# Kernel optimization log

Measured on AMD Instinct MI355X. Metric: run time of the kernel, lower is better.

Reference implementation:

```python
import jax, jax.numpy as jnp
import numpy as np

B, T, C = 8, 2048, 1024   # batch, seq_len, n_embd
HS = 1024                 # head_size


def setup_inputs() -> dict:
    key = jax.random.key(0)
    k1, k2, k3, k4 = jax.random.split(key, 4)
    x = jax.random.normal(k1, (B, T, C), dtype=jnp.float32)
    k_wei = jax.random.normal(k2, (C, HS), dtype=jnp.float32) * (C ** -0.5)
    q_wei = jax.random.normal(k3, (C, HS), dtype=jnp.float32) * (C ** -0.5)
    v_wei = jax.random.normal(k4, (C, HS), dtype=jnp.float32) * (C ** -0.5)
    mask = jnp.tril(jnp.ones((T, T), dtype=bool))  # causal tril, block_size >= T
    return {"x": x, "k_wei": k_wei, "q_wei": q_wei, "v_wei": v_wei, "mask": mask}


def reference(x, k_wei, q_wei, v_wei, mask):
    Bb, Tt, Cc = x.shape
    k = x @ k_wei                                   # [B,T,HS]
    q = x @ q_wei                                   # [B,T,HS]
    v = x @ v_wei                                   # [B,T,HS]
    # NOTE: source scales by C**-0.5 where C = n_embd (input channels)
    wei = jnp.einsum('bqh,bkh->bqk', q, k) * (Cc ** -0.5)  # [B,T,T]
    wei = jnp.where(mask[:Tt, :Tt], wei, -jnp.inf)
    wei = jax.nn.softmax(wei, axis=-1)
    out = wei @ v                                   # [B,T,HS]
    return out
```

## Files before the change

kernel.cpp:

```cpp
#include <hip/hip_runtime.h>
#include <hip/hip_bf16.h>
#include <stdint.h>

typedef __attribute__((ext_vector_type(4))) float f32x4;
typedef __attribute__((ext_vector_type(8))) short s16x8;

#define BARRIER() asm volatile("s_barrier" ::: "memory")
#define WAITV4()  asm volatile("s_waitcnt vmcnt(4)" ::: "memory")
#define WAITV0()  asm volatile("s_waitcnt vmcnt(0)" ::: "memory")
#define LGKM0()   asm volatile("s_waitcnt lgkmcnt(0)" ::: "memory")
#define MFMA(a, b, c) __builtin_amdgcn_mfma_f32_16x16x32_bf16((a), (b), (c), 0, 0, 0)

__device__ __forceinline__ ushort f2bf(float f) {
  union { float f; uint32_t u; } v; v.f = f;
  uint32_t r = v.u + 0x7FFFu + ((v.u >> 16) & 1u);
  return (ushort)(r >> 16);
}

__device__ __forceinline__ void gload_lds16(const ushort* g, short* l) {
  __builtin_amdgcn_global_load_lds(
      (const __attribute__((address_space(1))) uint32_t*)g,
      (__attribute__((address_space(3))) uint32_t*)l, 16, 0, 0);
}

__device__ __forceinline__ int xcd_swz(int flat, int q) {
  return (flat & 7) * q + (flat >> 3);
}

__device__ __forceinline__ void stage128(const ushort* __restrict__ g, int ld,
                                         int row0, int k0, short* lbase, int tid) {
  const int w  = tid >> 6;
  const int l  = tid & 63;
  const int lr = l >> 3;
  const int ls = l & 7;
  const ushort* gp = g + (size_t)(row0 + lr) * ld + k0 + ((ls ^ lr) << 3);
  short* lp = lbase + l * 8;
#pragma unroll
  for (int i = 0; i < 4; ++i) {
    const int R0 = w * 32 + i * 8;
    gload_lds16(gp + (size_t)R0 * ld, lp + R0 * 64);
  }
}

__device__ __forceinline__ void gstep(
    const ushort* __restrict__ A, int lda, const ushort* __restrict__ Bt, int ldb,
    int m0, int n0, int nk, int X, short* Ac, short* Bs,
    int tid, int s0, int aro, int bro, f32x4 acc[4][4], bool skipw)
{
  if (X + 1 < nk) { WAITV4(); } else { WAITV0(); }
  BARRIER();

  s16x8 b[4][2], a[4][2];
  if (!skipw) {
#pragma unroll
    for (int ni = 0; ni < 4; ++ni) {
      b[ni][0] = *(const s16x8*)(Bs + bro + ni * 1024 + s0);
      b[ni][1] = *(const s16x8*)(Bs + bro + ni * 1024 + (s0 ^ 32));
    }
#pragma unroll
    for (int mi = 0; mi < 4; ++mi) {
      a[mi][0] = *(const s16x8*)(Ac + aro + mi * 1024 + s0);
      a[mi][1] = *(const s16x8*)(Ac + aro + mi * 1024 + (s0 ^ 32));
    }
    __builtin_amdgcn_s_setprio(1);
#pragma unroll
    for (int mi = 0; mi < 2; ++mi)
#pragma unroll
      for (int ni = 0; ni < 4; ++ni) {
        acc[mi][ni] = MFMA(a[mi][0], b[ni][0], acc[mi][ni]);
        acc[mi][ni] = MFMA(a[mi][1], b[ni][1], acc[mi][ni]);
      }
    __builtin_amdgcn_s_setprio(0);
  }

  LGKM0();
  BARRIER();
  if (X + 1 < nk) stage128(Bt, ldb, n0, (X + 1) * 64, Bs, tid);
  if (X + 2 < nk) stage128(A, lda, m0, (X + 2) * 64, Ac, tid);
  if (!skipw) {
    __builtin_amdgcn_s_setprio(1);
#pragma unroll
    for (int mi = 0; mi < 2; ++mi)
#pragma unroll
      for (int ni = 0; ni < 4; ++ni) {
        acc[2 + mi][ni] = MFMA(a[2 + mi][0], b[ni][0], acc[2 + mi][ni]);
        acc[2 + mi][ni] = MFMA(a[2 + mi][1], b[ni][1], acc[2 + mi][ni]);
      }
    __builtin_amdgcn_s_setprio(0);
  }
}

__device__ __forceinline__ void gemm_core(
    const ushort* __restrict__ A, int lda, const ushort* __restrict__ Bt, int ldb,
    int m0, int n0, int nk, short* lds, f32x4 acc[4][4], bool skipw = false)
{
  const int tid  = threadIdx.x;
  const int lane = tid & 63, wid = tid >> 6;
  const int wr = wid >> 1, wc = wid & 1;
  const int fr = lane & 15, kg = lane >> 4;
  const int s0  = (kg ^ (fr & 7)) << 3;
  const int aro = (wr * 64 + fr) * 64;
  const int bro = (wc * 64 + fr) * 64;

  short* Ab0 = lds;
  short* Ab1 = lds + 8192;
  short* Bs  = lds + 16384;

#pragma unroll
  for (int i = 0; i < 4; ++i)
#pragma unroll
    for (int j = 0; j < 4; ++j)
      acc[i][j] = (f32x4){0.f, 0.f, 0.f, 0.f};

  stage128(A, lda, m0, 0, Ab0, tid);
  stage128(Bt, ldb, n0, 0, Bs, tid);
  if (nk > 1) stage128(A, lda, m0, 64, Ab1, tid);

#pragma unroll 1
  for (int X = 0; X < nk; X += 2) {
    gstep(A, lda, Bt, ldb, m0, n0, nk, X,     Ab0, Bs, tid, s0, aro, bro, acc, skipw);
    gstep(A, lda, Bt, ldb, m0, n0, nk, X + 1, Ab1, Bs, tid, s0, aro, bro, acc, skipw);
  }
}

__global__ void cvt_x(const float* __restrict__ x, ushort* __restrict__ xb)
{
  const size_t i = (size_t)(blockIdx.x * 256 + threadIdx.x) * 8;
  const f32x4 t0 = *(const f32x4*)(x + i);
  const f32x4 t1 = *(const f32x4*)(x + i + 4);
  uint4 pk;
  pk.x = (uint32_t)f2bf(t0[0]) | ((uint32_t)f2bf(t0[1]) << 16);
  pk.y = (uint32_t)f2bf(t0[2]) | ((uint32_t)f2bf(t0[3]) << 16);
  pk.z = (uint32_t)f2bf(t1[0]) | ((uint32_t)f2bf(t1[1]) << 16);
  pk.w = (uint32_t)f2bf(t1[2]) | ((uint32_t)f2bf(t1[3]) << 16);
  *(uint4*)(xb + i) = pk;
}

__global__ void cvt_w(const float* __restrict__ kw, const float* __restrict__ qw,
                      const float* __restrict__ vw, ushort* __restrict__ wt)
{
  __shared__ float t[32][33];
  const float* w = (blockIdx.z == 0) ? qw : (blockIdx.z == 1) ? kw : vw;
  const int n0 = blockIdx.x * 32, k0 = blockIdx.y * 32;
  t[threadIdx.y][threadIdx.x] = w[(size_t)(k0 + threadIdx.y) * 1024 + n0 + threadIdx.x];
  __syncthreads();
  wt[(size_t)blockIdx.z * 1048576 + (size_t)(n0 + threadIdx.y) * 1024 + k0 + threadIdx.x] =
      f2bf(t[threadIdx.x][threadIdx.y]);
}

__global__ __launch_bounds__(256) void gemm_qkv_impl(
    const ushort* __restrict__ xb, const ushort* __restrict__ wt,
    ushort* __restrict__ q, ushort* __restrict__ k, ushort* __restrict__ vT)
{
  extern __shared__ short lds[];
  const int flat = blockIdx.x + 24 * blockIdx.y;
  const int xcd = flat & 7, c = flat >> 3;
  const int mloc = c / 6, nloc = c - mloc * 6;
  const int m0 = ((xcd & 1) * 64 + mloc) * 128;
  const int n0 = ((xcd >> 1) * 6 + nloc) * 128;
  f32x4 acc[4][4];
  gemm_core(xb, 1024, wt, 1024, m0, n0, 16, lds, acc);

  const int tid  = threadIdx.x;
  const int lane = tid & 63;
  const int wid  = tid >> 6;
  const int wr = wid >> 1, wc = wid & 1;
  const int q4 = (lane >> 4) << 2;
  const int fr = lane & 15;
  const int z  = n0 >> 10;

  if (z < 2) {
    ushort* o = (z == 0) ? q : k;
    const int cb = (n0 & 1023) + wc * 64 + fr;
#pragma unroll
    for (int mi = 0; mi < 4; ++mi)
#pragma unroll
      for (int ni = 0; ni < 4; ++ni)
#pragma unroll
        for (int j = 0; j < 4; ++j) {
          const int r = m0 + wr * 64 + mi * 16 + q4 + j;
          o[(size_t)r * 1024 + cb + ni * 16] = f2bf(acc[mi][ni][j]);
        }
  } else {
    __syncthreads();
    ushort* tr = (ushort*)lds;
#pragma unroll
    for (int mi = 0; mi < 4; ++mi)
#pragma unroll
      for (int ni = 0; ni < 4; ++ni)
#pragma unroll
        for (int j = 0; j < 4; ++j) {
          const int cl = wc * 64 + ni * 16 + fr;
          const int rl = wr * 64 + mi * 16 + q4 + j;
          tr[cl * 136 + rl] = f2bf(acc[mi][ni][j]);
        }
    __syncthreads();
    const int cl   = tid >> 1;
    const int half = tid & 1;
    const ushort* src = tr + cl * 136 + half * 64;
    ushort* dst = vT + ((size_t)(m0 >> 11) * 1024 + (n0 & 1023) + cl) * 2048
                     + (m0 & 2047) + half * 64;
#pragma unroll
    for (int i = 0; i < 8; ++i)
      *(s16x8*)(dst + i * 8) = *(const s16x8*)(src + i * 8);
  }
}

__global__ __launch_bounds__(256) void gemm_sp(
    const ushort* __restrict__ q, const ushort* __restrict__ k,
    ushort* __restrict__ P, float* __restrict__ sums)
{
  extern __shared__ short lds[];
  const int nf = xcd_swz(blockIdx.x + 136 * blockIdx.z, 136);
  const int t  = nf % 136;
  const int b  = nf / 136;
  int qt = (int)((sqrtf(8.0f * (float)t + 1.0f) - 1.0f) * 0.5f);
  while ((qt + 1) * (qt + 2) / 2 <= t) ++qt;
  while (qt * (qt + 1) / 2 > t) --qt;
  const int kt = t - qt * (qt + 1) / 2;

  const int tid  = threadIdx.x;
  const int lane = tid & 63, wid = tid >> 6;
  const int wr = wid >> 1, wc = wid & 1;
  const int diag = (kt == qt);
  const bool skipw = diag && (wr == 0) && (wc == 1);

  f32x4 acc[4][4];
  const ushort* qb = q + (size_t)b * (2048 * 1024);
  const ushort* kb = k + (size_t)b * (2048 * 1024);
  gemm_core(qb, 1024, kb, 1024, qt * 128, kt * 128, 16, lds, acc, skipw);
  __syncthreads();
  float* rowsum = (float*)lds;

  const int q4 = (lane >> 4) << 2;
  const int fr = lane & 15;
  ushort* Pb = P + ((size_t)b << 22);

#pragma unroll
  for (int mi = 0; mi < 4; ++mi)
#pragma unroll
    for (int j = 0; j < 4; ++j) {
      const int rloc = wr * 64 + mi * 16 + q4 + j;
      const int rg   = qt * 128 + rloc;
      float s = 0.f;
#pragma unroll
      for (int ni = 0; ni < 4; ++ni) {
        const int cg = kt * 128 + wc * 64 + ni * 16 + fr;
        float e = __expf(acc[mi][ni][j] * 0.03125f - 10.f);
        if (diag && cg > rg) e = 0.f;
        s += e;
        Pb[(size_t)rg * 2048 + cg] = f2bf(e);
      }
#pragma unroll
      for (int m = 1; m < 16; m <<= 1) s += __shfl_xor(s, m);
      if (fr == 0) rowsum[wc * 128 + rloc] = s;
    }
  __syncthreads();
  if (tid < 128) {
    const float tot = rowsum[tid] + rowsum[128 + tid];
    atomicAdd(&sums[b * 2048 + qt * 128 + tid], tot);
  }
}

__global__ __launch_bounds__(256) void gemm_pv(
    const ushort* __restrict__ P, const ushort* __restrict__ vT,
    const float* __restrict__ sums, float* __restrict__ out)
{
  extern __shared__ short lds[];
  const int nf = xcd_swz(blockIdx.x + 8 * (blockIdx.y + 16 * blockIdx.z), 128);
  const int ht = nf & 7, qt = (nf >> 3) & 15, b = nf >> 7;
  f32x4 acc[4][4];
  const ushort* Pb = P  + ((size_t)b << 22);
  const ushort* Vb = vT + (size_t)b * (1024 * 2048);
  gemm_core(Pb, 2048, Vb, 2048, qt * 128, ht * 128, (qt + 1) * 2, lds, acc);

  float* ob = out + (size_t)b * 2097152;
  const int lane = threadIdx.x & 63;
  const int wid = threadIdx.x >> 6;
  const int wr = wid >> 1, wc = wid & 1;
  const int r0 = qt * 128 + wr * 64 + ((lane >> 4) << 2);
  const int c0 = ht * 128 + wc * 64 + (lane & 15);
#pragma unroll
  for (int mi = 0; mi < 4; ++mi)
#pragma unroll
    for (int j = 0; j < 4; ++j) {
      const int r = r0 + mi * 16 + j;
      const float inv = 1.0f / sums[b * 2048 + r];
#pragma unroll
      for (int ni = 0; ni < 4; ++ni)
        ob[(size_t)r * 1024 + (c0 + ni * 16)] = acc[mi][ni][j] * inv;
    }
}

extern "C" void kernel_launch(void* const* d_in, const int* in_sizes, int n_in,
                              void* d_out, int out_size, void* d_ws, size_t ws_size,
                              hipStream_t stream)
{
  const float* x  = (const float*)d_in[0];
  const float* kw = (const float*)d_in[1];
  const float* qw = (const float*)d_in[2];
  const float* vw = (const float*)d_in[3];
  float* out = (float*)d_out;
  char* ws = (char*)d_ws;

  ushort* xb   = (ushort*)ws;
  ushort* P    = (ushort*)ws;
  float*  sums = (float*)(ws + 67108864);
  ushort* wt   = (ushort*)(ws + 67174400);
  ushort* q    = (ushort*)(ws + 73465856);
  ushort* k    = (ushort*)(ws + 107020288);
  ushort* vT   = (ushort*)(ws + 140574720);

  const int LDSB = 49152;
  hipMemsetAsync(sums, 0, 8 * 2048 * sizeof(float), stream);
  cvt_x<<<8192, 256, 0, stream>>>(x, xb);
  cvt_w<<<dim3(32, 32, 3), dim3(32, 32), 0, stream>>>(kw, qw, vw, wt);
  gemm_qkv_impl<<<dim3(24, 128), 256, LDSB, stream>>>(xb, wt, q, k, vT);
  gemm_sp<<<dim3(136, 1, 8), 256, LDSB, stream>>>(q, k, P, sums);
  gemm_pv<<<dim3(8, 16, 8), 256, LDSB, stream>>>(P, vT, sums, out);
}
```

Measured before the change: 245.4 us.

## Fuse fp32-to-bf16 conversion of x into QKV GEMM A-tile loading

Drops the separate cvt_x kernel. The QKV GEMM now loads fp32 x directly into registers, converts it with the packed v_cvt_pk_bf16_f32 instruction, and writes bf16 into swizzled LDS double buffers. The loads are software-pipelined across the MFMA halves with explicit vmcnt waits. This removes one launch and the bf16 x round-trip through memory, but each GEMM tile now reads 2x more A bytes (fp32), and x is re-read across 24 column tiles, with higher register pressure.

```diff
diff --git a/kernel.cpp b/kernel.cpp
--- a/kernel.cpp
+++ b/kernel.cpp
@@ -6,6 +6,8 @@
 typedef __attribute__((ext_vector_type(8))) short s16x8;
 
 #define BARRIER() asm volatile("s_barrier" ::: "memory")
+#define WAITV12() asm volatile("s_waitcnt vmcnt(12)" ::: "memory")
+#define WAITV8()  asm volatile("s_waitcnt vmcnt(8)" ::: "memory")
 #define WAITV4()  asm volatile("s_waitcnt vmcnt(4)" ::: "memory")
 #define WAITV0()  asm volatile("s_waitcnt vmcnt(0)" ::: "memory")
 #define LGKM0()   asm volatile("s_waitcnt lgkmcnt(0)" ::: "memory")
@@ -15,6 +17,12 @@
   union { float f; uint32_t u; } v; v.f = f;
   uint32_t r = v.u + 0x7FFFu + ((v.u >> 16) & 1u);
   return (ushort)(r >> 16);
+}
+
+__device__ __forceinline__ uint32_t pk2(float lo, float hi) {
+  uint32_t r;
+  asm("v_cvt_pk_bf16_f32 %0, %1, %2" : "=v"(r) : "v"(lo), "v"(hi));
+  return r;
 }
 
 __device__ __forceinline__ void gload_lds16(const ushort* g, short* l) {
@@ -42,6 +50,7 @@
   }
 }
 
+
 __device__ __forceinline__ void gstep(
     const ushort* __restrict__ A, int lda, const ushort* __restrict__ Bt, int ldb,
     int m0, int n0, int nk, int X, short* Ac, short* Bs,
@@ -123,19 +132,6 @@
   }
 }
 
-__global__ void cvt_x(const float* __restrict__ x, ushort* __restrict__ xb)
-{
-  const size_t i = (size_t)(blockIdx.x * 256 + threadIdx.x) * 8;
-  const f32x4 t0 = *(const f32x4*)(x + i);
-  const f32x4 t1 = *(const f32x4*)(x + i + 4);
-  uint4 pk;
-  pk.x = (uint32_t)f2bf(t0[0]) | ((uint32_t)f2bf(t0[1]) << 16);
-  pk.y = (uint32_t)f2bf(t0[2]) | ((uint32_t)f2bf(t0[3]) << 16);
-  pk.z = (uint32_t)f2bf(t1[0]) | ((uint32_t)f2bf(t1[1]) << 16);
-  pk.w = (uint32_t)f2bf(t1[2]) | ((uint32_t)f2bf(t1[3]) << 16);
-  *(uint4*)(xb + i) = pk;
-}
-
 __global__ void cvt_w(const float* __restrict__ kw, const float* __restrict__ qw,
                       const float* __restrict__ vw, ushort* __restrict__ wt)
 {
@@ -148,8 +144,78 @@
       f2bf(t[threadIdx.x][threadIdx.y]);
 }
 
+
+#define ALOAD(rg, k0)                                                         \
+  {                                                                           \
+    const float* xp = x + (size_t)(m0 + lr) * 1024 + (k0) + ((ls ^ lr) << 3); \
+    _Pragma("unroll")                                                         \
+    for (int i = 0; i < 4; ++i) {                                             \
+      rg[2 * i]     = *(const f32x4*)(xp + (size_t)(w * 32 + i * 8) * 1024);  \
+      rg[2 * i + 1] = *(const f32x4*)(xp + (size_t)(w * 32 + i * 8) * 1024 + 4); \
+    }                                                                         \
+  }
+
+#define AWRITE(rg, Ab)                                                        \
+  {                                                                           \
+    _Pragma("unroll")                                                         \
+    for (int i = 0; i < 4; ++i) {                                             \
+      uint4 p;                                                                \
+      p.x = pk2(rg[2 * i][0], rg[2 * i][1]);                                  \
+      p.y = pk2(rg[2 * i][2], rg[2 * i][3]);                                  \
+      p.z = pk2(rg[2 * i + 1][0], rg[2 * i + 1][1]);                          \
+      p.w = pk2(rg[2 * i + 1][2], rg[2 * i + 1][3]);                          \
+      *(uint4*)((Ab) + ((size_t)(w * 32 + i * 8 + lr) * 64 + ls * 8)) = p;    \
+    }                                                                         \
+  }
+
+#define QSTEP(X, AbR, AbW, rCur, rNext)                                       \
+  {                                                                           \
+    s16x8 b[4][2], a[4][2];                                                   \
+    _Pragma("unroll")                                                         \
+    for (int ni = 0; ni < 4; ++ni) {                                          \
+      b[ni][0] = *(const s16x8*)(Bs + bro + ni * 1024 + s0);                  \
+      b[ni][1] = *(const s16x8*)(Bs + bro + ni * 1024 + (s0 ^ 32));           \
+    }                                                                         \
+    _Pragma("unroll")                                                         \
+    for (int mi = 0; mi < 4; ++mi) {                                          \
+      a[mi][0] = *(const s16x8*)((AbR) + aro + mi * 1024 + s0);               \
+      a[mi][1] = *(const s16x8*)((AbR) + aro + mi * 1024 + (s0 ^ 32));        \
+    }                                                                         \
+    __builtin_amdgcn_s_setprio(1);                                            \
+    _Pragma("unroll")                                                         \
+    for (int mi = 0; mi < 2; ++mi)                                            \
+      _Pragma("unroll")                                                       \
+      for (int ni = 0; ni < 4; ++ni) {                                        \
+        acc[mi][ni] = MFMA(a[mi][0], b[ni][0], acc[mi][ni]);                  \
+        acc[mi][ni] = MFMA(a[mi][1], b[ni][1], acc[mi][ni]);                  \
+      }                                                                       \
+    __builtin_amdgcn_s_setprio(0);                                            \
+    LGKM0();                                                                  \
+    BARRIER();                                                                \
+    if ((X) + 1 < 16) stage128(wt, 1024, n0, ((X) + 1) * 64, Bs, tid);        \
+    if ((X) + 2 < 16) ALOAD(rNext, ((X) + 2) * 64);                           \
+    if ((X) + 1 < 16) {                                                       \
+      if ((X) + 2 < 16) { WAITV12(); } else { WAITV4(); }                     \
+      AWRITE(rCur, AbW);                                                      \
+    }                                                                         \
+    __builtin_amdgcn_s_setprio(1);                                            \
+    _Pragma("unroll")                                                         \
+    for (int mi = 0; mi < 2; ++mi)                                            \
+      _Pragma("unroll")                                                       \
+      for (int ni = 0; ni < 4; ++ni) {                                        \
+        acc[2 + mi][ni] = MFMA(a[2 + mi][0], b[ni][0], acc[2 + mi][ni]);      \
+        acc[2 + mi][ni] = MFMA(a[2 + mi][1], b[ni][1], acc[2 + mi][ni]);      \
+      }                                                                       \
+    __builtin_amdgcn_s_setprio(0);                                            \
+    if ((X) + 1 < 16) {                                                       \
+      if ((X) + 2 < 16) { WAITV8(); } else { WAITV0(); }                      \
+      LGKM0();                                                                \
+      BARRIER();                                                              \
+    }                                                                         \
+  }
+
 __global__ __launch_bounds__(256) void gemm_qkv_impl(
-    const ushort* __restrict__ xb, const ushort* __restrict__ wt,
+    const float* __restrict__ x, const ushort* __restrict__ wt,
     ushort* __restrict__ q, ushort* __restrict__ k, ushort* __restrict__ vT)
 {
   extern __shared__ short lds[];
@@ -158,15 +224,44 @@
   const int mloc = c / 6, nloc = c - mloc * 6;
   const int m0 = ((xcd & 1) * 64 + mloc) * 128;
   const int n0 = ((xcd >> 1) * 6 + nloc) * 128;
+
+  const int tid  = threadIdx.x;
+  const int lane = tid & 63, wid = tid >> 6;
+  const int wr = wid >> 1, wc = wid & 1;
+  const int fr = lane & 15, kg = lane >> 4;
+  const int s0  = (kg ^ (fr & 7)) << 3;
+  const int aro = (wr * 64 + fr) * 64;
+  const int bro = (wc * 64 + fr) * 64;
+  const int w = tid >> 6, l = tid & 63, lr = l >> 3, ls = l & 7;
+
+  short* Ab0 = lds;
+  short* Ab1 = lds + 8192;
+  short* Bs  = lds + 16384;
+
   f32x4 acc[4][4];
-  gemm_core(xb, 1024, wt, 1024, m0, n0, 16, lds, acc);
-
-  const int tid  = threadIdx.x;
-  const int lane = tid & 63;
-  const int wid  = tid >> 6;
-  const int wr = wid >> 1, wc = wid & 1;
+#pragma unroll
+  for (int i = 0; i < 4; ++i)
+#pragma unroll
+    for (int j = 0; j < 4; ++j)
+      acc[i][j] = (f32x4){0.f, 0.f, 0.f, 0.f};
+
+  f32x4 rP[8], rQ[8];
+  ALOAD(rP, 0);
+  stage128(wt, 1024, n0, 0, Bs, tid);
+  ALOAD(rQ, 64);
+  WAITV12();
+  AWRITE(rP, Ab0);
+  WAITV8();
+  LGKM0();
+  BARRIER();
+
+#pragma unroll 1
+  for (int X = 0; X < 16; X += 2) {
+    QSTEP(X,     Ab0, Ab1, rQ, rP);
+    QSTEP(X + 1, Ab1, Ab0, rP, rQ);
+  }
+
   const int q4 = (lane >> 4) << 2;
-  const int fr = lane & 15;
   const int z  = n0 >> 10;
 
   if (z < 2) {
@@ -303,7 +398,6 @@
   float* out = (float*)d_out;
   char* ws = (char*)d_ws;
 
-  ushort* xb   = (ushort*)ws;
   ushort* P    = (ushort*)ws;
   float*  sums = (float*)(ws + 67108864);
   ushort* wt   = (ushort*)(ws + 67174400);
@@ -313,9 +407,8 @@
 
   const int LDSB = 49152;
   hipMemsetAsync(sums, 0, 8 * 2048 * sizeof(float), stream);
-  cvt_x<<<8192, 256, 0, stream>>>(x, xb);
   cvt_w<<<dim3(32, 32, 3), dim3(32, 32), 0, stream>>>(kw, qw, vw, wt);
-  gemm_qkv_impl<<<dim3(24, 128), 256, LDSB, stream>>>(xb, wt, q, k, vT);
+  gemm_qkv_impl<<<dim3(24, 128), 256, LDSB, stream>>>(x, wt, q, k, vT);
   gemm_sp<<<dim3(136, 1, 8), 256, LDSB, stream>>>(q, k, P, sums);
   gemm_pv<<<dim3(8, 16, 8), 256, LDSB, stream>>>(P, vT, sums, out);
 }
```

New measurement: 279.8 us. 14.0% more time.
